# Optimization experiments

Measured on AMD Instinct MI355X. Metric: run time of the kernel, lower is better.

## Reference

```python
import jax, jax.numpy as jnp
import numpy as np

EPS = 1e-5
NUM_GROUPS = 32

def _nin(x, w, b):
    # 1x1 conv: x (B,C,H,W), w (K,C), b (K,)
    return jnp.einsum('bchw,kc->bkhw', x, w) + b[None, :, None, None]

def _group_norm(x, gamma, beta, num_groups=NUM_GROUPS, eps=EPS):
    B, C, H, W = x.shape
    xg = x.reshape(B, num_groups, C // num_groups, H, W)
    mean = xg.mean(axis=(2, 3, 4), keepdims=True)
    var = xg.var(axis=(2, 3, 4), keepdims=True)
    xg = (xg - mean) * jax.lax.rsqrt(var + eps)
    x = xg.reshape(B, C, H, W)
    return x * gamma[None, :, None, None] + beta[None, :, None, None]

def setup_inputs() -> dict:
    key = jax.random.key(0)
    ks = jax.random.split(key, 10)
    B, C, H, W = 8, 512, 64, 64
    att = 512
    s = 0.02
    return {
        'x': jax.random.normal(ks[0], (B, C, H, W), dtype=jnp.float32),
        'gn_weight': jnp.ones((C,), jnp.float32),
        'gn_bias': jnp.zeros((C,), jnp.float32),
        'q_w': jax.random.normal(ks[1], (att, C), jnp.float32) * s,
        'q_b': jnp.zeros((att,), jnp.float32),
        'k_w': jax.random.normal(ks[2], (att, C), jnp.float32) * s,
        'k_b': jnp.zeros((att,), jnp.float32),
        'v_w': jax.random.normal(ks[3], (att, C), jnp.float32) * s,
        'v_b': jnp.zeros((att,), jnp.float32),
        'proj_w': jax.random.normal(ks[4], (C, att), jnp.float32) * s,
        'proj_b': jnp.zeros((C,), jnp.float32),
    }

def reference(x, gn_weight, gn_bias, q_w, q_b, k_w, k_b, v_w, v_b, proj_w, proj_b):
    B, C, H, W = x.shape
    h = _group_norm(x, gn_weight, gn_bias)
    q = _nin(h, q_w, q_b)  # (B, D, H, W)
    k = _nin(h, k_w, k_b)
    v = _nin(h, v_w, v_b)
    N = H * W
    qf = q.reshape(B, -1, N)
    kf = k.reshape(B, -1, N)
    vf = v.reshape(B, -1, N)
    scale = C ** (-0.5)  # note: scaled by input channel C, per source
    w = jnp.einsum('bdn,bdm->bnm', qf, kf) * scale  # (B, N, N)
    w = jax.nn.softmax(w, axis=-1)
    hf = jnp.einsum('bnm,bdm->bdn', w, vf)
    h = hf.reshape(B, -1, H, W)
    h = _nin(h, proj_w, proj_b)
    return x + h
```

## Files before the change

kernel.cpp:

```cpp
#include <hip/hip_runtime.h>
#include <hip/hip_bf16.h>
#include <cstdint>
#include <cstddef>

typedef __bf16 bf16_t;
typedef __bf16 bf16x8 __attribute__((ext_vector_type(8)));
typedef __bf16 bf16x4 __attribute__((ext_vector_type(4)));
typedef float f32x4 __attribute__((ext_vector_type(4)));

__device__ __forceinline__ void async16(const void* g, void* l) {
  __builtin_amdgcn_global_load_lds(
      (const __attribute__((address_space(1))) void*)g,
      (__attribute__((address_space(3))) void*)l,
      16, 0, 0);
}

__global__ __launch_bounds__(256) void f2b4(const float* __restrict__ w0,
                                            const float* __restrict__ w1,
                                            const float* __restrict__ w2,
                                            const float* __restrict__ w3,
                                            bf16_t* __restrict__ o0,
                                            bf16_t* __restrict__ o1,
                                            bf16_t* __restrict__ o2,
                                            bf16_t* __restrict__ o3) {
  const float* in = (blockIdx.y == 0) ? w0 : (blockIdx.y == 1) ? w1
                   : (blockIdx.y == 2) ? w2 : w3;
  bf16_t* out = (blockIdx.y == 0) ? o0 : (blockIdx.y == 1) ? o1
               : (blockIdx.y == 2) ? o2 : o3;
  const int i = blockIdx.x * 256 + threadIdx.x;
  float4 v = ((const float4*)in)[i];
  bf16x4 o = { (__bf16)v.x, (__bf16)v.y, (__bf16)v.z, (__bf16)v.w };
  ((bf16x4*)out)[i] = o;
}

__global__ __launch_bounds__(256) void groupnorm_t(const float* __restrict__ x,
                                                   const float* __restrict__ gamma,
                                                   const float* __restrict__ beta,
                                                   bf16_t* __restrict__ ht,
                                                   int b0) {
  const int g = blockIdx.x;
  const int lb = blockIdx.y;
  const int b = b0 + lb;
  const int t = threadIdx.x;
  const float* xg = x + ((size_t)(b * 512 + g * 16)) * 4096;
  const float4* x4 = (const float4*)xg;

  float s = 0.f, ss = 0.f;
  #pragma unroll 8
  for (int i = t; i < 16384; i += 256) {
    float4 v = x4[i];
    s  += (v.x + v.y) + (v.z + v.w);
    ss += (v.x * v.x + v.y * v.y) + (v.z * v.z + v.w * v.w);
  }
  #pragma unroll
  for (int o = 32; o; o >>= 1) { s += __shfl_xor(s, o); ss += __shfl_xor(ss, o); }
  __shared__ float rs[4], rss[4];
  if ((t & 63) == 0) { rs[t >> 6] = s; rss[t >> 6] = ss; }
  __syncthreads();
  const float S  = (rs[0] + rs[1]) + (rs[2] + rs[3]);
  const float SS = (rss[0] + rss[1]) + (rss[2] + rss[3]);
  const float inv_n = 1.0f / 65536.0f;
  const float mean = S * inv_n;
  const float var  = SS * inv_n - mean * mean;
  const float rstd = rsqrtf(var + 1e-5f);

  float ga[16], be[16];
  #pragma unroll
  for (int cc = 0; cc < 16; cc++) {
    const float gm = gamma[g * 16 + cc] * rstd;
    ga[cc] = gm;
    be[cc] = beta[g * 16 + cc] - mean * gm;
  }

  bf16_t* hg = ht + (size_t)lb * 4096 * 512 + g * 16;
  for (int n = t; n < 4096; n += 256) {
    bf16_t o[16];
    #pragma unroll
    for (int cc = 0; cc < 16; cc++)
      o[cc] = (bf16_t)(xg[(size_t)cc * 4096 + n] * ga[cc] + be[cc]);
    bf16x8* dst = (bf16x8*)(hg + (size_t)n * 512);
    dst[0] = *(bf16x8*)&o[0];
    dst[1] = *(bf16x8*)&o[8];
  }
}

__global__ __launch_bounds__(256) void softmax_row_bf16(bf16_t* __restrict__ SP) {
  const int row = blockIdx.x;
  const int t = threadIdx.x;
  bf16_t* base = SP + (size_t)blockIdx.y * 4096 * 4096 + (size_t)row * 4096;
  bf16x8* R = (bf16x8*)base + t * 2;

  float v[16];
  bf16x8 a = R[0], b = R[1];
  #pragma unroll
  for (int i = 0; i < 8; i++) { v[i] = (float)a[i]; v[8 + i] = (float)b[i]; }

  float m = -3.0e38f;
  #pragma unroll
  for (int i = 0; i < 16; i++) m = fmaxf(m, v[i]);
  #pragma unroll
  for (int o = 32; o; o >>= 1) m = fmaxf(m, __shfl_xor(m, o));
  __shared__ float rm[4], rsum[4];
  if ((t & 63) == 0) rm[t >> 6] = m;
  __syncthreads();
  m = fmaxf(fmaxf(rm[0], rm[1]), fmaxf(rm[2], rm[3]));

  float s = 0.f;
  #pragma unroll
  for (int i = 0; i < 16; i++) { v[i] = __expf(v[i] - m); s += v[i]; }
  #pragma unroll
  for (int o = 32; o; o >>= 1) s += __shfl_xor(s, o);
  if ((t & 63) == 0) rsum[t >> 6] = s;
  __syncthreads();
  s = (rsum[0] + rsum[1]) + (rsum[2] + rsum[3]);
  const float inv = 1.0f / s;

  #pragma unroll
  for (int i = 0; i < 8; i++) { a[i] = (__bf16)(v[i] * inv); b[i] = (__bf16)(v[8 + i] * inv); }
  R[0] = a; R[1] = b;
}

template <int OUTF32, int BIAS_MODE, int RESID, int SWAP>
__global__ __launch_bounds__(256)
void gemm_bt(const bf16_t* __restrict__ A, const bf16_t* __restrict__ B,
             void* __restrict__ Cv, const float* __restrict__ bias,
             const float* __restrict__ resid,
             int TM, int TN, int Z, int K, float scale,
             long sA, long sB, long sC, long sR) {
  __shared__ alignas(16) bf16_t lA[4096];
  __shared__ alignas(16) bf16_t lB[4096];

  const int lid = blockIdx.x;
  const int xcd = lid & 7;
  const int j   = lid >> 3;
  const int sd  = SWAP ? TN : TM;
  const int I   = SWAP ? TM : TN;
  const int spx = (sd * Z) >> 3;
  const int strip = xcd * spx + j / I;
  const int inner = j % I;
  const int z    = strip / sd;
  const int sidx = strip % sd;
  const int bm = (SWAP ? inner : sidx) * 128;
  const int bn = (SWAP ? sidx : inner) * 128;
  const int N = TN * 128;

  const int t = threadIdx.x;
  const int lane = t & 63;
  const int w = t >> 6;
  const int wm = (w >> 1) * 64;
  const int wn = (w & 1) * 64;
  const bf16_t* Ab = A + (size_t)z * (size_t)sA;
  const bf16_t* Bb = B + (size_t)z * (size_t)sB;

  const int lrow = lane >> 2;
  const int lcol = (lane & 3) * 8;
  const int quad = lane >> 4;
  const int l15 = lane & 15;

  const bf16_t* gA0 = Ab + (size_t)(bm + w * 16 + lrow) * K + lcol;
  const bf16_t* gA1 = Ab + (size_t)(bm + (w + 4) * 16 + lrow) * K + lcol;
  const bf16_t* gB0 = Bb + (size_t)(bn + w * 16 + lrow) * K + lcol;
  const bf16_t* gB1 = Bb + (size_t)(bn + (w + 4) * 16 + lrow) * K + lcol;
  bf16_t* lA0 = &lA[w * 512];
  bf16_t* lA1 = &lA[(w + 4) * 512];
  bf16_t* lB0 = &lB[w * 512];
  bf16_t* lB1 = &lB[(w + 4) * 512];

  f32x4 acc[4][4] = {};

  for (int k0 = 0; k0 < K; k0 += 32) {
    __syncthreads();
    async16(gA0 + k0, lA0);
    async16(gA1 + k0, lA1);
    async16(gB0 + k0, lB0);
    async16(gB1 + k0, lB1);
    __syncthreads();

    bf16x8 af[4], bfr[4];
    #pragma unroll
    for (int i = 0; i < 4; i++) {
      af[i]  = *(const bf16x8*)&lA[(wm + i * 16 + l15) * 32 + quad * 8];
      bfr[i] = *(const bf16x8*)&lB[(wn + i * 16 + l15) * 32 + quad * 8];
    }
    #pragma unroll
    for (int i = 0; i < 4; i++)
      #pragma unroll
      for (int jj = 0; jj < 4; jj++)
        acc[i][jj] = __builtin_amdgcn_mfma_f32_16x16x32_bf16(af[i], bfr[jj],
                                                             acc[i][jj], 0, 0, 0);
  }

  float* Cf = (float*)Cv + (size_t)z * (size_t)sC;
  bf16_t* Cb = (bf16_t*)Cv + (size_t)z * (size_t)sC;
  const float* Rb = RESID ? (resid + (size_t)z * (size_t)sR) : nullptr;

  #pragma unroll
  for (int i = 0; i < 4; i++) {
    const int row0 = bm + wm + i * 16 + quad * 4;
    #pragma unroll
    for (int jj = 0; jj < 4; jj++) {
      const int col = bn + wn + jj * 16 + l15;
      #pragma unroll
      for (int r = 0; r < 4; r++) {
        float v = acc[i][jj][r] * scale;
        const int row = row0 + r;
        if (BIAS_MODE == 1) v += bias[row];
        else if (BIAS_MODE == 2) v += bias[col];
        const size_t idx = (size_t)row * N + col;
        if (RESID) v += Rb[idx];
        if (OUTF32) Cf[idx] = v;
        else Cb[idx] = (bf16_t)v;
      }
    }
  }
}

extern "C" void kernel_launch(void* const* d_in, const int* in_sizes, int n_in,
                              void* d_out, int out_size, void* d_ws, size_t ws_size,
                              hipStream_t stream) {
  const float* x   = (const float*)d_in[0];
  const float* gnw = (const float*)d_in[1];
  const float* gnb = (const float*)d_in[2];
  const float* qw  = (const float*)d_in[3];
  const float* qb  = (const float*)d_in[4];
  const float* kw  = (const float*)d_in[5];
  const float* kb  = (const float*)d_in[6];
  const float* vw  = (const float*)d_in[7];
  const float* vb  = (const float*)d_in[8];
  const float* pw  = (const float*)d_in[9];
  const float* pb  = (const float*)d_in[10];
  float* out = (float*)d_out;

  char* ws = (char*)d_ws;
  size_t off = 0;
  auto alloc = [&](size_t bytes) -> void* {
    void* p = ws + off;
    off += (bytes + 255) & ~(size_t)255;
    return p;
  };

  const long sND  = 4096L * 512;
  const long sNN  = 4096L * 4096;

  bf16_t* wqb = (bf16_t*)alloc(512ull * 512 * 2);
  bf16_t* wkb = (bf16_t*)alloc(512ull * 512 * 2);
  bf16_t* wvb = (bf16_t*)alloc(512ull * 512 * 2);
  bf16_t* wpb = (bf16_t*)alloc(512ull * 512 * 2);
  bf16_t* ht  = (bf16_t*)alloc(4ull * 4096 * 512 * 2);
  bf16_t* qbf = (bf16_t*)alloc(4ull * 4096 * 512 * 2);
  bf16_t* kbf = (bf16_t*)alloc(4ull * 4096 * 512 * 2);
  bf16_t* vbf = (bf16_t*)alloc(4ull * 4096 * 512 * 2);
  bf16_t* SP  = (bf16_t*)alloc(4ull * 4096 * 4096 * 2);
  bf16_t* hfb = ht;

  f2b4<<<dim3(256, 4), 256, 0, stream>>>(qw, kw, vw, pw, wqb, wkb, wvb, wpb);

  const float scale = 0.044194173824159216f;

  for (int b0 = 0; b0 < 8; b0 += 4) {
    const size_t xoff = (size_t)b0 * 512 * 4096;

    groupnorm_t<<<dim3(32, 4), 256, 0, stream>>>(x, gnw, gnb, ht, b0);

    gemm_bt<0, 2, 0, 0><<<512, 256, 0, stream>>>(
        ht, wqb, qbf, qb, nullptr, 32, 4, 4, 512, 1.0f, sND, 0, sND, 0);
    gemm_bt<0, 2, 0, 0><<<512, 256, 0, stream>>>(
        ht, wkb, kbf, kb, nullptr, 32, 4, 4, 512, 1.0f, sND, 0, sND, 0);
    gemm_bt<0, 1, 0, 1><<<512, 256, 0, stream>>>(
        wvb, ht, vbf, vb, nullptr, 4, 32, 4, 512, 1.0f, 0, sND, sND, 0);

    gemm_bt<0, 0, 0, 0><<<4096, 256, 0, stream>>>(
        qbf, kbf, SP, nullptr, nullptr, 32, 32, 4, 512, scale, sND, sND, sNN, 0);

    softmax_row_bf16<<<dim3(4096, 4), 256, 0, stream>>>(SP);

    gemm_bt<0, 0, 0, 0><<<512, 256, 0, stream>>>(
        SP, vbf, hfb, nullptr, nullptr, 32, 4, 4, 4096, 1.0f, sNN, sND, sND, 0);

    gemm_bt<1, 1, 1, 1><<<512, 256, 0, stream>>>(
        wpb, hfb, out + xoff, pb, x + xoff, 4, 32, 4, 512, 1.0f, 0, sND, sND, sND);
  }
}
```

Before: 819.6 us.

## Fuse QK^T, softmax and PV into a flash-attention kernel over all batches

Replaces the QK^T GEMM, the separate row softmax and the PV GEMM with a single fused MFMA kernel. Scores stay in registers and LDS, and normalisation by the running row sum is deferred to the end. This removes the full 4096x4096 bf16 score matrix round trips through HBM. The batch-of-4 loop is also dropped so groupnorm and the projections run over all 8 batches in one launch each, at the cost of larger workspace buffers. The softmax skips max subtraction, which can overflow exp for inputs with large logits.

```diff
diff --git a/kernel.cpp b/kernel.cpp
--- a/kernel.cpp
+++ b/kernel.cpp
@@ -36,11 +36,9 @@
 __global__ __launch_bounds__(256) void groupnorm_t(const float* __restrict__ x,
                                                    const float* __restrict__ gamma,
                                                    const float* __restrict__ beta,
-                                                   bf16_t* __restrict__ ht,
-                                                   int b0) {
+                                                   bf16_t* __restrict__ ht) {
   const int g = blockIdx.x;
-  const int lb = blockIdx.y;
-  const int b = b0 + lb;
+  const int b = blockIdx.y;
   const int t = threadIdx.x;
   const float* xg = x + ((size_t)(b * 512 + g * 16)) * 4096;
   const float4* x4 = (const float4*)xg;
@@ -72,7 +70,7 @@
     be[cc] = beta[g * 16 + cc] - mean * gm;
   }
 
-  bf16_t* hg = ht + (size_t)lb * 4096 * 512 + g * 16;
+  bf16_t* hg = ht + (size_t)b * 4096 * 512 + g * 16;
   for (int n = t; n < 4096; n += 256) {
     bf16_t o[16];
     #pragma unroll
@@ -82,42 +80,6 @@
     dst[0] = *(bf16x8*)&o[0];
     dst[1] = *(bf16x8*)&o[8];
   }
-}
-
-__global__ __launch_bounds__(256) void softmax_row_bf16(bf16_t* __restrict__ SP) {
-  const int row = blockIdx.x;
-  const int t = threadIdx.x;
-  bf16_t* base = SP + (size_t)blockIdx.y * 4096 * 4096 + (size_t)row * 4096;
-  bf16x8* R = (bf16x8*)base + t * 2;
-
-  float v[16];
-  bf16x8 a = R[0], b = R[1];
-  #pragma unroll
-  for (int i = 0; i < 8; i++) { v[i] = (float)a[i]; v[8 + i] = (float)b[i]; }
-
-  float m = -3.0e38f;
-  #pragma unroll
-  for (int i = 0; i < 16; i++) m = fmaxf(m, v[i]);
-  #pragma unroll
-  for (int o = 32; o; o >>= 1) m = fmaxf(m, __shfl_xor(m, o));
-  __shared__ float rm[4], rsum[4];
-  if ((t & 63) == 0) rm[t >> 6] = m;
-  __syncthreads();
-  m = fmaxf(fmaxf(rm[0], rm[1]), fmaxf(rm[2], rm[3]));
-
-  float s = 0.f;
-  #pragma unroll
-  for (int i = 0; i < 16; i++) { v[i] = __expf(v[i] - m); s += v[i]; }
-  #pragma unroll
-  for (int o = 32; o; o >>= 1) s += __shfl_xor(s, o);
-  if ((t & 63) == 0) rsum[t >> 6] = s;
-  __syncthreads();
-  s = (rsum[0] + rsum[1]) + (rsum[2] + rsum[3]);
-  const float inv = 1.0f / s;
-
-  #pragma unroll
-  for (int i = 0; i < 8; i++) { a[i] = (__bf16)(v[i] * inv); b[i] = (__bf16)(v[8 + i] * inv); }
-  R[0] = a; R[1] = b;
 }
 
 template <int OUTF32, int BIAS_MODE, int RESID, int SWAP>
@@ -213,6 +175,122 @@
       }
     }
   }
+}
+
+__global__ __launch_bounds__(256, 2)
+void flash_attn(const bf16_t* __restrict__ Qm, const bf16_t* __restrict__ Km,
+                const bf16_t* __restrict__ Vm, bf16_t* __restrict__ Om,
+                float scale) {
+  __shared__ alignas(16) bf16_t lK[2][128][32];
+  __shared__ alignas(16) bf16_t lV[256][32];
+  __shared__ alignas(16) bf16_t lS[4][16][136];
+
+  const int bid = blockIdx.x;
+  const int z = bid & 7;
+  const int qb = bid >> 3;
+  const int m0 = qb * 64;
+
+  const int t = threadIdx.x;
+  const int lane = t & 63;
+  const int w = t >> 6;
+  const int quad = lane >> 4;
+  const int l15 = lane & 15;
+  const int krow = lane >> 2;
+  const int kcol = (lane & 3) * 8;
+
+  const size_t sND = 4096ull * 512;
+  const bf16_t* q = Qm + z * sND;
+  const bf16_t* k = Km + z * sND;
+  const bf16_t* v = Vm + z * sND;
+
+  bf16x8 qf[16];
+  {
+    const bf16_t* qrow = q + (size_t)(m0 + w * 16 + l15) * 512 + quad * 8;
+    #pragma unroll
+    for (int kk = 0; kk < 16; kk++)
+      qf[kk] = *(const bf16x8*)(qrow + kk * 32);
+  }
+
+  f32x4 o_acc[32] = {};
+  float l_run[4] = {0.f, 0.f, 0.f, 0.f};
+
+  for (int kc = 0; kc < 4096; kc += 128) {
+    f32x4 s_acc[8] = {};
+    #pragma unroll
+    for (int kk2 = 0; kk2 < 8; kk2++) {
+      __syncthreads();
+      #pragma unroll
+      for (int c = 0; c < 2; c++)
+        #pragma unroll
+        for (int half = 0; half < 2; half++) {
+          const bf16_t* g = k + (size_t)(kc + w * 16 + c * 64 + krow) * 512
+                              + kk2 * 64 + half * 32 + kcol;
+          bf16_t* l = &lK[half][w * 16 + c * 64][0] + krow * 32 + kcol;
+          async16(g, l);
+        }
+      __syncthreads();
+      #pragma unroll
+      for (int kkh = 0; kkh < 2; kkh++)
+        #pragma unroll
+        for (int n = 0; n < 8; n++) {
+          bf16x8 kf = *(const bf16x8*)&lK[kkh][n * 16 + l15][quad * 8];
+          s_acc[n] = __builtin_amdgcn_mfma_f32_16x16x32_bf16(
+              qf[kk2 * 2 + kkh], kf, s_acc[n], 0, 0, 0);
+        }
+    }
+
+    float lsum[4] = {0.f, 0.f, 0.f, 0.f};
+    #pragma unroll
+    for (int n = 0; n < 8; n++)
+      #pragma unroll
+      for (int r = 0; r < 4; r++) {
+        float e = __expf(s_acc[n][r] * scale);
+        lsum[r] += e;
+        lS[w][quad * 4 + r][n * 16 + l15] = (bf16_t)e;
+      }
+    #pragma unroll
+    for (int r = 0; r < 4; r++) {
+      float s = lsum[r];
+      s += __shfl_xor(s, 1); s += __shfl_xor(s, 2);
+      s += __shfl_xor(s, 4); s += __shfl_xor(s, 8);
+      l_run[r] += s;
+    }
+
+    for (int kks = 0; kks < 4; kks++) {
+      #pragma unroll
+      for (int dh = 0; dh < 2; dh++) {
+        __syncthreads();
+        #pragma unroll
+        for (int c = 0; c < 4; c++) {
+          const bf16_t* g = v + (size_t)(dh * 256 + w * 16 + c * 64 + krow) * 4096
+                              + kc + kks * 32 + kcol;
+          bf16_t* l = &lV[w * 16 + c * 64][0] + krow * 32 + kcol;
+          async16(g, l);
+        }
+        __syncthreads();
+        bf16x8 af = *(const bf16x8*)&lS[w][l15][kks * 32 + quad * 8];
+        #pragma unroll
+        for (int nd = 0; nd < 16; nd++) {
+          bf16x8 vf = *(const bf16x8*)&lV[nd * 16 + l15][quad * 8];
+          o_acc[dh * 16 + nd] = __builtin_amdgcn_mfma_f32_16x16x32_bf16(
+              af, vf, o_acc[dh * 16 + nd], 0, 0, 0);
+        }
+      }
+    }
+  }
+
+  bf16_t* o = Om + z * sND;
+  float rl[4];
+  #pragma unroll
+  for (int r = 0; r < 4; r++) rl[r] = 1.0f / l_run[r];
+  #pragma unroll
+  for (int nd = 0; nd < 32; nd++)
+    #pragma unroll
+    for (int r = 0; r < 4; r++) {
+      const int row = m0 + w * 16 + quad * 4 + r;
+      const int col = nd * 16 + l15;
+      o[(size_t)row * 512 + col] = (bf16_t)(o_acc[nd][r] * rl[r]);
+    }
 }
 
 extern "C" void kernel_launch(void* const* d_in, const int* in_sizes, int n_in,
@@ -239,45 +317,31 @@
     return p;
   };
 
-  const long sND  = 4096L * 512;
-  const long sNN  = 4096L * 4096;
+  const long sND = 4096L * 512;
 
   bf16_t* wqb = (bf16_t*)alloc(512ull * 512 * 2);
   bf16_t* wkb = (bf16_t*)alloc(512ull * 512 * 2);
   bf16_t* wvb = (bf16_t*)alloc(512ull * 512 * 2);
   bf16_t* wpb = (bf16_t*)alloc(512ull * 512 * 2);
-  bf16_t* ht  = (bf16_t*)alloc(4ull * 4096 * 512 * 2);
-  bf16_t* qbf = (bf16_t*)alloc(4ull * 4096 * 512 * 2);
-  bf16_t* kbf = (bf16_t*)alloc(4ull * 4096 * 512 * 2);
-  bf16_t* vbf = (bf16_t*)alloc(4ull * 4096 * 512 * 2);
-  bf16_t* SP  = (bf16_t*)alloc(4ull * 4096 * 4096 * 2);
+  bf16_t* ht  = (bf16_t*)alloc(8ull * 4096 * 512 * 2);
+  bf16_t* qbf = (bf16_t*)alloc(8ull * 4096 * 512 * 2);
+  bf16_t* kbf = (bf16_t*)alloc(8ull * 4096 * 512 * 2);
+  bf16_t* vbf = (bf16_t*)alloc(8ull * 4096 * 512 * 2);
   bf16_t* hfb = ht;
 
   f2b4<<<dim3(256, 4), 256, 0, stream>>>(qw, kw, vw, pw, wqb, wkb, wvb, wpb);
+  groupnorm_t<<<dim3(32, 8), 256, 0, stream>>>(x, gnw, gnb, ht);
+
+  gemm_bt<0, 2, 0, 0><<<1024, 256, 0, stream>>>(
+      ht, wqb, qbf, qb, nullptr, 32, 4, 8, 512, 1.0f, sND, 0, sND, 0);
+  gemm_bt<0, 2, 0, 0><<<1024, 256, 0, stream>>>(
+      ht, wkb, kbf, kb, nullptr, 32, 4, 8, 512, 1.0f, sND, 0, sND, 0);
+  gemm_bt<0, 1, 0, 1><<<1024, 256, 0, stream>>>(
+      wvb, ht, vbf, vb, nullptr, 4, 32, 8, 512, 1.0f, 0, sND, sND, 0);
 
   const float scale = 0.044194173824159216f;
-
-  for (int b0 = 0; b0 < 8; b0 += 4) {
-    const size_t xoff = (size_t)b0 * 512 * 4096;
-
-    groupnorm_t<<<dim3(32, 4), 256, 0, stream>>>(x, gnw, gnb, ht, b0);
-
-    gemm_bt<0, 2, 0, 0><<<512, 256, 0, stream>>>(
-        ht, wqb, qbf, qb, nullptr, 32, 4, 4, 512, 1.0f, sND, 0, sND, 0);
-    gemm_bt<0, 2, 0, 0><<<512, 256, 0, stream>>>(
-        ht, wkb, kbf, kb, nullptr, 32, 4, 4, 512, 1.0f, sND, 0, sND, 0);
-    gemm_bt<0, 1, 0, 1><<<512, 256, 0, stream>>>(
-        wvb, ht, vbf, vb, nullptr, 4, 32, 4, 512, 1.0f, 0, sND, sND, 0);
-
-    gemm_bt<0, 0, 0, 0><<<4096, 256, 0, stream>>>(
-        qbf, kbf, SP, nullptr, nullptr, 32, 32, 4, 512, scale, sND, sND, sNN, 0);
-
-    softmax_row_bf16<<<dim3(4096, 4), 256, 0, stream>>>(SP);
-
-    gemm_bt<0, 0, 0, 0><<<512, 256, 0, stream>>>(
-        SP, vbf, hfb, nullptr, nullptr, 32, 4, 4, 4096, 1.0f, sNN, sND, sND, 0);
-
-    gemm_bt<1, 1, 1, 1><<<512, 256, 0, stream>>>(
-        wpb, hfb, out + xoff, pb, x + xoff, 4, 32, 4, 512, 1.0f, 0, sND, sND, sND);
-  }
-}
+  flash_attn<<<512, 256, 0, stream>>>(qbf, kbf, vbf, hfb, scale);
+
+  gemm_bt<1, 1, 1, 1><<<1024, 256, 0, stream>>>(
+      wpb, hfb, out, pb, x, 4, 32, 8, 512, 1.0f, 0, sND, 512L * 4096, 512L * 4096);
+}
```

After: 834.3 us. No clear change (+1.8%).
